# Kernel optimization log

Hardware: AMD Instinct MI355X
Metric: run time of the kernel (lower is better)

## Reference

```python
import jax, jax.numpy as jnp
import numpy as np

IGNORE_INDEX = -100
BETA = 0.1
B, S, H, V = 8, 512, 4096, 32000


def setup_inputs() -> dict:
    key = jax.random.key(0)
    k1, k2, k3 = jax.random.split(key, 3)
    x = jax.random.normal(k1, (B, S, H), dtype=jnp.float32)
    weight = jax.random.normal(k2, (V, H), dtype=jnp.float32) * 0.02
    target = jax.random.randint(k3, (B, S), 0, V, dtype=jnp.int32)
    return {"x": x, "weight": weight, "target": target}


def reference(x, weight, target):
    len_chosen = x.shape[0] // 2
    # fused linear head: logits [B, S, V]
    logits = jnp.einsum('bsh,vh->bsv', x, weight)
    # log-softmax in fp32 as in the torch module (dtype=torch.float32)
    log_probs = jax.nn.log_softmax(logits.astype(jnp.float32), axis=-1)
    safe_tgt = jnp.clip(target, 0, V - 1)
    per_token_logps = jnp.take_along_axis(log_probs, safe_tgt[..., None].astype(jnp.int32), axis=-1)[..., 0]
    loss_mask = target != IGNORE_INDEX
    per_token_logps = jnp.where(loss_mask, per_token_logps, 0.0)
    seq_logps = per_token_logps.sum(-1)  # [B]
    # average_log_prob=True: divide by number of non-masked tokens
    seq_logps = seq_logps / loss_mask.sum(-1).astype(jnp.float32)
    policy_chosen_logps = seq_logps[:len_chosen]
    policy_rejected_logps = seq_logps[len_chosen:]
    # logits means accumulated across chunks == global means
    chosen_logits_mean = logits[:len_chosen].mean()
    rejected_logits_mean = logits[len_chosen:].mean()
    # use_ref_model=False -> reference logps are zeros
    ref_chosen = jnp.zeros_like(policy_chosen_logps)
    ref_rejected = jnp.zeros_like(policy_rejected_logps)
    # DPO preference loss
    logits_diff = BETA * ((policy_chosen_logps - ref_chosen) - (policy_rejected_logps - ref_rejected))
    preference_loss = -jax.nn.log_sigmoid(logits_diff).sum() / len_chosen
    nll_loss = jnp.zeros(())  # compute_nll_loss=False
    loss = 1.0 * nll_loss + preference_loss
    return (loss, policy_chosen_logps, policy_rejected_logps,
            chosen_logits_mean, rejected_logits_mean, nll_loss)
```

## Files before the change

kernel.cpp:

```cpp
#include <hip/hip_runtime.h>
#include <hip/hip_bf16.h>
#include <math.h>

#define IGNORE_INDEX (-100)
#define BETA 0.1f

constexpr int Mdim = 8 * 512;
constexpr int Kdim = 4096;
constexpr int Ndim = 32000;
constexpr int BM = 128, BN = 128;
constexpr int BK8 = 128;
constexpr int MT = Mdim / BM;
constexpr int NT = Ndim / BN;

typedef __bf16 bf16x8 __attribute__((ext_vector_type(8)));
typedef __bf16 bf16x4 __attribute__((ext_vector_type(4)));
typedef float  floatx4 __attribute__((ext_vector_type(4)));
typedef int    v8i __attribute__((ext_vector_type(8)));
typedef int    v4i __attribute__((ext_vector_type(4)));

#define GPTR(p) ((const __attribute__((address_space(1))) void*)(p))
#define LPTR(p) ((__attribute__((address_space(3))) void*)(p))

__global__ void cvt_f32_fp8(const float4* __restrict__ src, uint* __restrict__ dst, long n4) {
    long stride = (long)gridDim.x * blockDim.x;
    for (long i = (long)blockIdx.x * blockDim.x + threadIdx.x; i < n4; i += stride) {
        float4 a = src[i];
        int r = __builtin_amdgcn_cvt_pk_fp8_f32(a.x, a.y, 0, false);
        r     = __builtin_amdgcn_cvt_pk_fp8_f32(a.z, a.w, r, true);
        dst[i] = (uint)r;
    }
}

__global__ __launch_bounds__(256, 2)
void dpo_gemm_fp8(const unsigned char* __restrict__ x8, const unsigned char* __restrict__ w8,
                  const int* __restrict__ target,
                  float* __restrict__ sumexp, float* __restrict__ sumlog,
                  float* __restrict__ tgtlogit)
{
    __shared__ unsigned char As[BM * BK8];
    __shared__ unsigned char Bs[BN * BK8];
    __shared__ int tgt_s[BM];

    const int tid  = threadIdx.x;
    const int lane = tid & 63;
    const int wid  = tid >> 6;
    const int wm   = wid & 1;
    const int wn   = wid >> 1;
    const int bid  = blockIdx.x;
    const int m0   = (bid & (MT - 1)) * BM;
    const int n0   = (bid / MT) * BN;

    if (tid < BM) tgt_s[tid] = target[m0 + tid];

    floatx4 acc[4][4] = {};

    const int qr = lane >> 4;
    const int cr = lane & 15;

    const int srow   = lane >> 3;
    const int schunk = (lane & 7) ^ srow;
    const unsigned char* xg = x8 + (size_t)(m0 + wid * 8 + srow) * Kdim + schunk * 16;
    const unsigned char* wg = w8 + (size_t)(n0 + wid * 8 + srow) * Kdim + schunk * 16;
    unsigned char* As_w = As + wid * 1024;
    unsigned char* Bs_w = Bs + wid * 1024;

    for (int k0 = 0; k0 < Kdim; k0 += BK8) {
        __syncthreads();
        #pragma unroll
        for (int i = 0; i < 4; ++i) {
            __builtin_amdgcn_global_load_lds(GPTR(xg + k0 + (size_t)i * 32 * Kdim),
                                             LPTR(As_w + i * 4096), 16, 0, 0);
            __builtin_amdgcn_global_load_lds(GPTR(wg + k0 + (size_t)i * 32 * Kdim),
                                             LPTR(Bs_w + i * 4096), 16, 0, 0);
        }
        __syncthreads();

        const int s  = cr & 7;
        const int c0 = (2 * qr) ^ s;
        const int c1 = (2 * qr + 1) ^ s;

        v8i afrag[4], bfrag[4];
        #pragma unroll
        for (int mi = 0; mi < 4; ++mi) {
            const int base = (wm * 64 + mi * 16 + cr) * BK8;
            v4i lo = *(const v4i*)&As[base + c0 * 16];
            v4i hi = *(const v4i*)&As[base + c1 * 16];
            afrag[mi] = __builtin_shufflevector(lo, hi, 0, 1, 2, 3, 4, 5, 6, 7);
        }
        #pragma unroll
        for (int ni = 0; ni < 4; ++ni) {
            const int base = (wn * 64 + ni * 16 + cr) * BK8;
            v4i lo = *(const v4i*)&Bs[base + c0 * 16];
            v4i hi = *(const v4i*)&Bs[base + c1 * 16];
            bfrag[ni] = __builtin_shufflevector(lo, hi, 0, 1, 2, 3, 4, 5, 6, 7);
        }

        #pragma unroll
        for (int mi = 0; mi < 4; ++mi)
            #pragma unroll
            for (int ni = 0; ni < 4; ++ni)
                acc[mi][ni] = __builtin_amdgcn_mfma_scale_f32_16x16x128_f8f6f4(
                    afrag[mi], bfrag[ni], acc[mi][ni],
                    0 , 0 ,
                    0, 0x7F7F7F7F,
                    0, 0x7F7F7F7F);
    }

    #pragma unroll
    for (int mi = 0; mi < 4; ++mi) {
        #pragma unroll
        for (int reg = 0; reg < 4; ++reg) {
            const int lrow = wm * 64 + mi * 16 + qr * 4 + reg;
            const int grow = m0 + lrow;
            const int t = tgt_s[lrow];
            float se = 0.f, sl = 0.f;
            #pragma unroll
            for (int ni = 0; ni < 4; ++ni) {
                float v = acc[mi][ni][reg];
                int gcol = n0 + wn * 64 + ni * 16 + cr;
                if (t == gcol) tgtlogit[grow] = v;
                se += __expf(v);
                sl += v;
            }
            #pragma unroll
            for (int st = 1; st < 16; st <<= 1) {
                se += __shfl_xor(se, st, 64);
                sl += __shfl_xor(sl, st, 64);
            }
            if (cr == 0) {
                atomicAdd(&sumexp[grow], se);
                atomicAdd(&sumlog[grow], sl);
            }
        }
    }
}

__global__ __launch_bounds__(256, 2)
void dpo_gemm_f32(const float* __restrict__ x, const float* __restrict__ w,
                  const int* __restrict__ target,
                  float* __restrict__ sumexp, float* __restrict__ sumlog,
                  float* __restrict__ tgtlogit)
{
    constexpr int BK = 32;
    constexpr int LDA = 40;
    __shared__ __bf16 As[BM * LDA];
    __shared__ __bf16 Bs[BN * LDA];
    __shared__ int tgt_s[BM];

    const int tid  = threadIdx.x;
    const int lane = tid & 63;
    const int wid  = tid >> 6;
    const int wm   = wid & 1;
    const int wn   = wid >> 1;
    const int bid  = blockIdx.x;
    const int m0   = (bid & (MT - 1)) * BM;
    const int n0   = (bid / MT) * BN;

    if (tid < BM) tgt_s[tid] = target[m0 + tid];

    floatx4 acc[4][4] = {};
    const int qr = lane >> 4;
    const int cr = lane & 15;

    for (int k0 = 0; k0 < Kdim; k0 += BK) {
        __syncthreads();
        #pragma unroll
        for (int i = 0; i < 4; ++i) {
            int idx = tid + i * 256;
            int row = idx >> 3;
            int c4  = (idx & 7) * 4;
            float4 v = *(const float4*)(x + (size_t)(m0 + row) * Kdim + k0 + c4);
            bf16x4 p;
            p[0] = (__bf16)v.x; p[1] = (__bf16)v.y; p[2] = (__bf16)v.z; p[3] = (__bf16)v.w;
            *(bf16x4*)&As[row * LDA + c4] = p;
        }
        #pragma unroll
        for (int i = 0; i < 4; ++i) {
            int idx = tid + i * 256;
            int row = idx >> 3;
            int c4  = (idx & 7) * 4;
            float4 v = *(const float4*)(w + (size_t)(n0 + row) * Kdim + k0 + c4);
            bf16x4 p;
            p[0] = (__bf16)v.x; p[1] = (__bf16)v.y; p[2] = (__bf16)v.z; p[3] = (__bf16)v.w;
            *(bf16x4*)&Bs[row * LDA + c4] = p;
        }
        __syncthreads();

        bf16x8 afrag[4], bfrag[4];
        #pragma unroll
        for (int mi = 0; mi < 4; ++mi)
            afrag[mi] = *(const bf16x8*)&As[(wm * 64 + mi * 16 + cr) * LDA + qr * 8];
        #pragma unroll
        for (int ni = 0; ni < 4; ++ni)
            bfrag[ni] = *(const bf16x8*)&Bs[(wn * 64 + ni * 16 + cr) * LDA + qr * 8];

        #pragma unroll
        for (int mi = 0; mi < 4; ++mi)
            #pragma unroll
            for (int ni = 0; ni < 4; ++ni)
                acc[mi][ni] = __builtin_amdgcn_mfma_f32_16x16x32_bf16(
                    afrag[mi], bfrag[ni], acc[mi][ni], 0, 0, 0);
    }

    #pragma unroll
    for (int mi = 0; mi < 4; ++mi) {
        #pragma unroll
        for (int reg = 0; reg < 4; ++reg) {
            const int lrow = wm * 64 + mi * 16 + qr * 4 + reg;
            const int grow = m0 + lrow;
            const int t = tgt_s[lrow];
            float se = 0.f, sl = 0.f;
            #pragma unroll
            for (int ni = 0; ni < 4; ++ni) {
                float v = acc[mi][ni][reg];
                int gcol = n0 + wn * 64 + ni * 16 + cr;
                if (t == gcol) tgtlogit[grow] = v;
                se += __expf(v);
                sl += v;
            }
            #pragma unroll
            for (int st = 1; st < 16; st <<= 1) {
                se += __shfl_xor(se, st, 64);
                sl += __shfl_xor(sl, st, 64);
            }
            if (cr == 0) {
                atomicAdd(&sumexp[grow], se);
                atomicAdd(&sumlog[grow], sl);
            }
        }
    }
}

__global__ void dpo_finalize(const float* __restrict__ sumexp,
                             const float* __restrict__ sumlog,
                             const float* __restrict__ tgtlogit,
                             const int* __restrict__ target,
                             float* __restrict__ out)
{
    __shared__ float s_logp[8], s_sl[8];
    const int lane = threadIdx.x & 63;
    const int w    = threadIdx.x >> 6;

    float lp = 0.f, cnt = 0.f, sl = 0.f;
    #pragma unroll
    for (int i = 0; i < 8; ++i) {
        int t  = w * 512 + i * 64 + lane;
        int tg = target[t];
        if (tg != IGNORE_INDEX) {
            lp  += tgtlogit[t] - logf(sumexp[t]);
            cnt += 1.f;
        }
        sl += sumlog[t];
    }
    #pragma unroll
    for (int s = 1; s < 64; s <<= 1) {
        lp  += __shfl_xor(lp, s, 64);
        cnt += __shfl_xor(cnt, s, 64);
        sl  += __shfl_xor(sl, s, 64);
    }
    if (lane == 0) { s_logp[w] = lp / cnt; s_sl[w] = sl; }
    __syncthreads();

    if (threadIdx.x == 0) {
        float cm = 0.f, rm = 0.f, loss = 0.f;
        for (int i = 0; i < 4; ++i) { cm += s_sl[i]; rm += s_sl[4 + i]; }
        const float denom = 4.f * 512.f * 32000.f;
        cm /= denom; rm /= denom;
        for (int i = 0; i < 4; ++i) {
            float d = BETA * (s_logp[i] - s_logp[4 + i]);
            float l = (d > 0.f) ? log1pf(expf(-d)) : (-d + log1pf(expf(d)));
            loss += l;
        }
        loss *= 0.25f;
        out[0] = loss;
        for (int i = 0; i < 4; ++i) out[1 + i] = s_logp[i];
        for (int i = 0; i < 4; ++i) out[5 + i] = s_logp[4 + i];
        out[9]  = cm;
        out[10] = rm;
        out[11] = 0.f;
    }
}

extern "C" void kernel_launch(void* const* d_in, const int* in_sizes, int n_in,
                              void* d_out, int out_size, void* d_ws, size_t ws_size,
                              hipStream_t stream) {
    const float* x      = (const float*)d_in[0];
    const float* wgt    = (const float*)d_in[1];
    const int*   target = (const int*)d_in[2];
    float* out = (float*)d_out;

    float* sumexp   = (float*)d_ws;
    float* sumlog   = sumexp + Mdim;
    float* tgtlogit = sumlog + Mdim;
    char*  base     = (char*)d_ws + 3 * Mdim * sizeof(float);
    unsigned char* x8 = (unsigned char*)base;
    unsigned char* w8 = x8 + (size_t)Mdim * Kdim;

    const size_t ws_needed = 3 * Mdim * sizeof(float)
                           + (size_t)Mdim * Kdim
                           + (size_t)Ndim * Kdim;

    hipMemsetAsync(d_ws, 0, 2 * Mdim * sizeof(float), stream);

    if (ws_size >= ws_needed) {
        const long nx4 = (long)Mdim * Kdim / 4;
        const long nw4 = (long)Ndim * Kdim / 4;
        int bx = (int)(((nx4 + 255) / 256) < 2048 ? ((nx4 + 255) / 256) : 2048);
        int bw = (int)(((nw4 + 255) / 256) < 2048 ? ((nw4 + 255) / 256) : 2048);
        cvt_f32_fp8<<<bx, 256, 0, stream>>>((const float4*)x,   (uint*)x8, nx4);
        cvt_f32_fp8<<<bw, 256, 0, stream>>>((const float4*)wgt, (uint*)w8, nw4);
        dpo_gemm_fp8<<<MT * NT, 256, 0, stream>>>(x8, w8, target, sumexp, sumlog, tgtlogit);
    } else {
        dpo_gemm_f32<<<MT * NT, 256, 0, stream>>>(x, wgt, target, sumexp, sumlog, tgtlogit);
    }
    dpo_finalize<<<1, 512, 0, stream>>>(sumexp, sumlog, tgtlogit, target, out);
}
```

Before: 1.408 ms.

## Enlarge FP8 GEMM tiles to 256x256 with double-buffered LDS and grid swizzle

The FP8 logits GEMM now uses 256x256 block tiles with 512 threads, and each wave computes a 128x64 sub-tile. This raises operand reuse per LDS load and cuts global traffic per output. The K loop double-buffers LDS: loads for the next tile are issued between the fragment reads of the current tile, so there is one barrier per iteration instead of two. It also adds a block-index swizzle for better L2 locality and s_setprio around the MFMA bursts. The cost is about 128KB of LDS per block, which allows only one block per CU and raises accumulator register pressure.

```diff
diff --git a/kernel.cpp b/kernel.cpp
--- a/kernel.cpp
+++ b/kernel.cpp
@@ -8,8 +8,13 @@
 constexpr int Mdim = 8 * 512;
 constexpr int Kdim = 4096;
 constexpr int Ndim = 32000;
+
+constexpr int BM2 = 256, BN2 = 256, BK8 = 128;
+constexpr int MT2 = Mdim / BM2;
+constexpr int NT2 = Ndim / BN2;
+constexpr int NTILES = Kdim / BK8;
+
 constexpr int BM = 128, BN = 128;
-constexpr int BK8 = 128;
 constexpr int MT = Mdim / BM;
 constexpr int NT = Ndim / BN;
 
@@ -32,93 +37,137 @@
     }
 }
 
-__global__ __launch_bounds__(256, 2)
+__global__ __launch_bounds__(512, 2)
 void dpo_gemm_fp8(const unsigned char* __restrict__ x8, const unsigned char* __restrict__ w8,
                   const int* __restrict__ target,
                   float* __restrict__ sumexp, float* __restrict__ sumlog,
                   float* __restrict__ tgtlogit)
 {
-    __shared__ unsigned char As[BM * BK8];
-    __shared__ unsigned char Bs[BN * BK8];
-    __shared__ int tgt_s[BM];
+    __shared__ unsigned char Alds[2 * BM2 * BK8];
+    __shared__ unsigned char Blds[2 * BN2 * BK8];
+    __shared__ int tgt_s[BM2];
 
     const int tid  = threadIdx.x;
     const int lane = tid & 63;
     const int wid  = tid >> 6;
-    const int wm   = wid & 1;
-    const int wn   = wid >> 1;
-    const int bid  = blockIdx.x;
-    const int m0   = (bid & (MT - 1)) * BM;
-    const int n0   = (bid / MT) * BN;
-
-    if (tid < BM) tgt_s[tid] = target[m0 + tid];
-
-    floatx4 acc[4][4] = {};
+    const int wr   = wid >> 2;
+    const int wc   = wid & 3;
+
+    const int bid = blockIdx.x;
+    const int swz = (bid & 7) * (MT2 * NT2 / 8) + (bid >> 3);
+    const int m0  = (swz & (MT2 - 1)) * BM2;
+    const int n0  = (swz / MT2) * BN2;
+
+    if (tid < BM2) tgt_s[tid] = target[m0 + tid];
+
+    floatx4 acc[8][4] = {};
 
     const int qr = lane >> 4;
     const int cr = lane & 15;
 
     const int srow   = lane >> 3;
     const int schunk = (lane & 7) ^ srow;
-    const unsigned char* xg = x8 + (size_t)(m0 + wid * 8 + srow) * Kdim + schunk * 16;
-    const unsigned char* wg = w8 + (size_t)(n0 + wid * 8 + srow) * Kdim + schunk * 16;
-    unsigned char* As_w = As + wid * 1024;
-    unsigned char* Bs_w = Bs + wid * 1024;
-
-    for (int k0 = 0; k0 < Kdim; k0 += BK8) {
-        __syncthreads();
-        #pragma unroll
-        for (int i = 0; i < 4; ++i) {
-            __builtin_amdgcn_global_load_lds(GPTR(xg + k0 + (size_t)i * 32 * Kdim),
-                                             LPTR(As_w + i * 4096), 16, 0, 0);
-            __builtin_amdgcn_global_load_lds(GPTR(wg + k0 + (size_t)i * 32 * Kdim),
-                                             LPTR(Bs_w + i * 4096), 16, 0, 0);
-        }
-        __syncthreads();
-
-        const int s  = cr & 7;
-        const int c0 = (2 * qr) ^ s;
-        const int c1 = (2 * qr + 1) ^ s;
-
-        v8i afrag[4], bfrag[4];
+    const unsigned char* xg = x8 + (size_t)(m0 + wid * 32 + srow) * Kdim + schunk * 16;
+    const unsigned char* wg = w8 + (size_t)(n0 + wid * 32 + srow) * Kdim + schunk * 16;
+    const int stage_base = wid * 32 * BK8;
+
+    #pragma unroll
+    for (int i = 0; i < 4; ++i) {
+        __builtin_amdgcn_global_load_lds(GPTR(xg + (size_t)i * 8 * Kdim),
+                                         LPTR(Alds + stage_base + i * 1024), 16, 0, 0);
+        __builtin_amdgcn_global_load_lds(GPTR(wg + (size_t)i * 8 * Kdim),
+                                         LPTR(Blds + stage_base + i * 1024), 16, 0, 0);
+    }
+    __syncthreads();
+
+    const int sx = cr & 7;
+    const int c0 = (2 * qr) ^ sx;
+    const int c1 = (2 * qr + 1) ^ sx;
+
+    for (int t = 0; t < NTILES; ++t) {
+        const int s = t & 1;
+        const unsigned char* Asl = Alds + s * (BM2 * BK8);
+        const unsigned char* Bsl = Blds + s * (BN2 * BK8);
+        unsigned char* Asn = (unsigned char*)Alds + (s ^ 1) * (BM2 * BK8) + stage_base;
+        unsigned char* Bsn = (unsigned char*)Blds + (s ^ 1) * (BN2 * BK8) + stage_base;
+
+        v8i bfrag[4];
+        #pragma unroll
+        for (int ni = 0; ni < 4; ++ni) {
+            const int base = (wc * 64 + ni * 16 + cr) * BK8;
+            v4i lo = *(const v4i*)&Bsl[base + c0 * 16];
+            v4i hi = *(const v4i*)&Bsl[base + c1 * 16];
+            bfrag[ni] = __builtin_shufflevector(lo, hi, 0, 1, 2, 3, 4, 5, 6, 7);
+        }
+
+        if (t + 1 < NTILES) {
+            const unsigned char* g = xg + (size_t)(t + 1) * BK8;
+            #pragma unroll
+            for (int i = 0; i < 4; ++i)
+                __builtin_amdgcn_global_load_lds(GPTR(g + (size_t)i * 8 * Kdim),
+                                                 LPTR(Asn + i * 1024), 16, 0, 0);
+        }
+
+        v8i afrag[4];
         #pragma unroll
         for (int mi = 0; mi < 4; ++mi) {
-            const int base = (wm * 64 + mi * 16 + cr) * BK8;
-            v4i lo = *(const v4i*)&As[base + c0 * 16];
-            v4i hi = *(const v4i*)&As[base + c1 * 16];
+            const int base = (wr * 128 + mi * 16 + cr) * BK8;
+            v4i lo = *(const v4i*)&Asl[base + c0 * 16];
+            v4i hi = *(const v4i*)&Asl[base + c1 * 16];
             afrag[mi] = __builtin_shufflevector(lo, hi, 0, 1, 2, 3, 4, 5, 6, 7);
         }
-        #pragma unroll
-        for (int ni = 0; ni < 4; ++ni) {
-            const int base = (wn * 64 + ni * 16 + cr) * BK8;
-            v4i lo = *(const v4i*)&Bs[base + c0 * 16];
-            v4i hi = *(const v4i*)&Bs[base + c1 * 16];
-            bfrag[ni] = __builtin_shufflevector(lo, hi, 0, 1, 2, 3, 4, 5, 6, 7);
-        }
-
+
+        if (t + 1 < NTILES) {
+            const unsigned char* g = wg + (size_t)(t + 1) * BK8;
+            #pragma unroll
+            for (int i = 0; i < 4; ++i)
+                __builtin_amdgcn_global_load_lds(GPTR(g + (size_t)i * 8 * Kdim),
+                                                 LPTR(Bsn + i * 1024), 16, 0, 0);
+        }
+
+        __builtin_amdgcn_s_setprio(1);
         #pragma unroll
         for (int mi = 0; mi < 4; ++mi)
             #pragma unroll
             for (int ni = 0; ni < 4; ++ni)
                 acc[mi][ni] = __builtin_amdgcn_mfma_scale_f32_16x16x128_f8f6f4(
                     afrag[mi], bfrag[ni], acc[mi][ni],
-                    0 , 0 ,
-                    0, 0x7F7F7F7F,
-                    0, 0x7F7F7F7F);
-    }
-
-    #pragma unroll
-    for (int mi = 0; mi < 4; ++mi) {
+                    0, 0, 0, 0x7F7F7F7F, 0, 0x7F7F7F7F);
+        __builtin_amdgcn_s_setprio(0);
+
+        #pragma unroll
+        for (int mi = 0; mi < 4; ++mi) {
+            const int base = (wr * 128 + 64 + mi * 16 + cr) * BK8;
+            v4i lo = *(const v4i*)&Asl[base + c0 * 16];
+            v4i hi = *(const v4i*)&Asl[base + c1 * 16];
+            afrag[mi] = __builtin_shufflevector(lo, hi, 0, 1, 2, 3, 4, 5, 6, 7);
+        }
+
+        __builtin_amdgcn_s_setprio(1);
+        #pragma unroll
+        for (int mi = 0; mi < 4; ++mi)
+            #pragma unroll
+            for (int ni = 0; ni < 4; ++ni)
+                acc[4 + mi][ni] = __builtin_amdgcn_mfma_scale_f32_16x16x128_f8f6f4(
+                    afrag[mi], bfrag[ni], acc[4 + mi][ni],
+                    0, 0, 0, 0x7F7F7F7F, 0, 0x7F7F7F7F);
+        __builtin_amdgcn_s_setprio(0);
+
+        __syncthreads();
+    }
+
+    #pragma unroll
+    for (int mi8 = 0; mi8 < 8; ++mi8) {
         #pragma unroll
         for (int reg = 0; reg < 4; ++reg) {
-            const int lrow = wm * 64 + mi * 16 + qr * 4 + reg;
+            const int lrow = wr * 128 + mi8 * 16 + qr * 4 + reg;
             const int grow = m0 + lrow;
             const int t = tgt_s[lrow];
             float se = 0.f, sl = 0.f;
             #pragma unroll
             for (int ni = 0; ni < 4; ++ni) {
-                float v = acc[mi][ni][reg];
-                int gcol = n0 + wn * 64 + ni * 16 + cr;
+                float v = acc[mi8][ni][reg];
+                int gcol = n0 + wc * 64 + ni * 16 + cr;
                 if (t == gcol) tgtlogit[grow] = v;
                 se += __expf(v);
                 sl += v;
@@ -310,7 +359,7 @@
         int bw = (int)(((nw4 + 255) / 256) < 2048 ? ((nw4 + 255) / 256) : 2048);
         cvt_f32_fp8<<<bx, 256, 0, stream>>>((const float4*)x,   (uint*)x8, nx4);
         cvt_f32_fp8<<<bw, 256, 0, stream>>>((const float4*)wgt, (uint*)w8, nw4);
-        dpo_gemm_fp8<<<MT * NT, 256, 0, stream>>>(x8, w8, target, sumexp, sumlog, tgtlogit);
+        dpo_gemm_fp8<<<MT2 * NT2, 512, 0, stream>>>(x8, w8, target, sumexp, sumlog, tgtlogit);
     } else {
         dpo_gemm_f32<<<MT * NT, 256, 0, stream>>>(x, wgt, target, sumexp, sumlog, tgtlogit);
     }
```

New measurement: 1.309 ms. -7.1%, faster.
